# Kernel tuning notes

Measured on AMD Instinct MI355X. Metric: run time of the kernel, lower is better.

The kernel has to match this reference:

```python
import jax, jax.numpy as jnp
import numpy as np

NUM_HEADS = 12
HEAD_DIM = 64  # hidden 768 / 12


def setup_inputs() -> dict:
    key = jax.random.key(0)
    k1, k2, k3, k4 = jax.random.split(key, 4)
    B, S, H = 8, 1024, 768
    scale = 1.0 / np.sqrt(H)
    hidden_states = jax.random.normal(k1, (B, S, H), dtype=jnp.float32)
    Wq = jax.random.normal(k2, (H, H), dtype=jnp.float32) * scale
    Wk = jax.random.normal(k3, (H, H), dtype=jnp.float32) * scale
    Wv = jax.random.normal(k4, (H, H), dtype=jnp.float32) * scale
    return {"hidden_states": hidden_states, "Wq": Wq, "Wk": Wk, "Wv": Wv}


def reference(hidden_states, Wq, Wk, Wv):
    B, S, H = hidden_states.shape
    nh, hd = NUM_HEADS, HEAD_DIM
    # Linear projections, no bias. torch Linear: x @ W.T with W of shape [out, in];
    # here weights are stored [out, in] == [H, H].
    def proj(W):
        y = jnp.einsum('bsh,oh->bso', hidden_states, W)
        return y.reshape(B, S, nh, hd).transpose(0, 2, 1, 3)  # [B, nh, S, hd]
    q = proj(Wq)
    k = proj(Wk)
    v = proj(Wv)
    scale = 1.0 / np.sqrt(hd).astype(np.float32)
    scores = jnp.einsum('bhqd,bhkd->bhqk', q, k) * scale  # [B, nh, S, S]
    probs = jax.nn.softmax(scores, axis=-1)
    ctx = jnp.einsum('bhqk,bhkd->bhqd', probs, v)  # [B, nh, S, hd]
    ctx = ctx.transpose(0, 2, 1, 3).reshape(B, S, nh * hd)  # [B, S, H]
    return ctx
```

## Files before the change

### kernel.cpp

```cpp
#include <hip/hip_runtime.h>
#include <hip/hip_fp16.h>

typedef _Float16 f16;
typedef _Float16 f16x2 __attribute__((ext_vector_type(2)));
typedef _Float16 f16x4 __attribute__((ext_vector_type(4)));
typedef _Float16 f16x8 __attribute__((ext_vector_type(8)));
typedef float f32x4 __attribute__((ext_vector_type(4)));

#define GLB_AS __attribute__((address_space(1)))
#define LDS_AS __attribute__((address_space(3)))

__device__ __forceinline__ void gload_lds16(const f16* g, f16* lds) {
    __builtin_amdgcn_global_load_lds((const GLB_AS uint32_t*)g,
                                     (LDS_AS uint32_t*)lds, 16, 0, 0);
}

__device__ __forceinline__ int swz(int r, int c8) {
    return r * 64 + (((c8) ^ (r & 7)) << 3);
}

__global__ void cvt_all(const float* __restrict__ hs, const float* __restrict__ wq,
                        const float* __restrict__ wk, const float* __restrict__ wv,
                        f16* __restrict__ hs16, f16* __restrict__ w16) {
    int i = blockIdx.x * 256 + threadIdx.x;
    const float4* src;
    f16x4* dst;
    int off;
    if (i < 1572864) {
        src = (const float4*)hs; dst = (f16x4*)hs16; off = i;
    } else {
        int j = i - 1572864;
        int w = j / 147456;
        off = j - w * 147456;
        src = (const float4*)(w == 0 ? wq : (w == 1 ? wk : wv));
        dst = (f16x4*)(w16 + (size_t)w * 589824);
    }
    float4 v = src[off];
    f16x4 h = {(f16)v.x, (f16)v.y, (f16)v.z, (f16)v.w};
    dst[off] = h;
}

#define QSCALE 0.18033688011112043f

__global__ __launch_bounds__(256, 3) void qkv_gemm(
        const f16* __restrict__ A, const f16* __restrict__ W,
        f16* __restrict__ Qh, f16* __restrict__ Kh, f16* __restrict__ Vth) {
    __shared__ f16 As[128 * 64];
    __shared__ f16 Bs[128 * 64];
    const int m0 = blockIdx.x * 128;
    const int n0 = blockIdx.y * 128;
    const int tid = threadIdx.x;
    const int wave = tid >> 6, lane = tid & 63;
    const int wm = wave & 1, wn = wave >> 1;
    const int quad = lane >> 4, l16 = lane & 15;
    const int srow = lane >> 3;
    const int scol = (((lane & 7) ^ srow) << 3);

    f32x4 acc[4][4] = {};

    const f16* Abase = A + (size_t)m0 * 768;
    const f16* Wbase = W + (size_t)n0 * 768;

    for (int kt = 0; kt < 12; ++kt) {
        const int k0 = kt * 64;
        __syncthreads();
#pragma unroll
        for (int j = 0; j < 4; ++j) {
            int inst = wave * 4 + j;
            int row = inst * 8 + srow;
            gload_lds16(Abase + (size_t)row * 768 + k0 + scol, &As[inst * 512]);
            gload_lds16(Wbase + (size_t)row * 768 + k0 + scol, &Bs[inst * 512]);
        }
        __syncthreads();
#pragma unroll
        for (int kk = 0; kk < 2; ++kk) {
            f16x8 af[4], bf[4];
#pragma unroll
            for (int mi = 0; mi < 4; ++mi) {
                int r = wm * 64 + mi * 16 + l16;
                af[mi] = *(const f16x8*)&As[swz(r, kk * 4 + quad)];
            }
#pragma unroll
            for (int ni = 0; ni < 4; ++ni) {
                int r = wn * 64 + ni * 16 + l16;
                bf[ni] = *(const f16x8*)&Bs[swz(r, kk * 4 + quad)];
            }
#pragma unroll
            for (int mi = 0; mi < 4; ++mi)
#pragma unroll
                for (int ni = 0; ni < 4; ++ni)
                    acc[mi][ni] = __builtin_amdgcn_mfma_f32_16x16x32_f16(
                        af[mi], bf[ni], acc[mi][ni], 0, 0, 0);
        }
    }

    const int seg = n0 / 768;
    const int obase = n0 - seg * 768;
    const float scale = (seg == 0) ? QSCALE : 1.0f;
#pragma unroll
    for (int mi = 0; mi < 4; ++mi) {
#pragma unroll
        for (int ni = 0; ni < 4; ++ni) {
            int o = obase + wn * 64 + ni * 16 + l16;
            int h = o >> 6, d = o & 63;
            if (seg == 2) {
                int gm0 = m0 + wm * 64 + mi * 16 + quad * 4;
                int b = gm0 >> 10, s = gm0 & 1023;
                size_t bh = (size_t)(b * 12 + h);
                f16x4 v4 = {(f16)acc[mi][ni][0], (f16)acc[mi][ni][1],
                            (f16)acc[mi][ni][2], (f16)acc[mi][ni][3]};
                *(f16x4*)&Vth[(bh << 16) + ((size_t)d << 10) + s] = v4;
            } else {
                f16* dst = (seg == 0) ? Qh : Kh;
#pragma unroll
                for (int r = 0; r < 4; ++r) {
                    int gm = m0 + wm * 64 + mi * 16 + quad * 4 + r;
                    int b = gm >> 10, s = gm & 1023;
                    size_t bh = (size_t)(b * 12 + h);
                    dst[((bh << 10 | s) << 6) + d] = (f16)(acc[mi][ni][r] * scale);
                }
            }
        }
    }
}

__global__ __launch_bounds__(256, 3) void attn(
        const f16* __restrict__ Qh, const f16* __restrict__ Kh,
        const f16* __restrict__ Vth, float* __restrict__ out) {
    __shared__ f16 QsPt[128 * 64];
    __shared__ f16 Ks[2][64 * 64];
    __shared__ f16 Vts[2][64 * 64];
    const int bh = blockIdx.x;
    const int q0 = blockIdx.y * 128;
    const int b = bh / 12, h = bh % 12;
    const int tid = threadIdx.x, wave = tid >> 6, lane = tid & 63;
    const int quad = lane >> 4, l16 = lane & 15;
    const int srow = lane >> 3;
    const int scol = (((lane & 7) ^ srow) << 3);

    const f16* qbase = Qh + ((size_t)bh * 1024 + q0) * 64;
    const f16* kbase = Kh + (size_t)bh * 1024 * 64;
    const f16* vtbase = Vth + (size_t)bh * 64 * 1024;

#pragma unroll
    for (int j = 0; j < 4; ++j) {
        int inst = wave * 4 + j;
        int row = inst * 8 + srow;
        gload_lds16(qbase + row * 64 + scol, &QsPt[inst * 512]);
    }
#pragma unroll
    for (int j = 0; j < 2; ++j) {
        int inst = wave * 2 + j;
        int row = inst * 8 + srow;
        gload_lds16(kbase + (size_t)row * 64 + scol, &Ks[0][inst * 512]);
        gload_lds16(vtbase + (size_t)row * 1024 + scol, &Vts[0][inst * 512]);
    }
    __syncthreads();

    f16x8 qa[2][2];
#pragma unroll
    for (int t = 0; t < 2; ++t)
#pragma unroll
        for (int kk = 0; kk < 2; ++kk)
            qa[t][kk] = *(const f16x8*)&QsPt[swz(wave * 32 + t * 16 + l16, kk * 4 + quad)];
    __syncthreads();

    const int ptb0 = (wave * 2 + 0) * 1024;
    const int ptb1 = (wave * 2 + 1) * 1024;
    const int rowoff = l16 * 64;

    f32x4 o_acc[2][4] = {};
    float rsum[2] = {0.f, 0.f};

    for (int kb = 0; kb < 16; ++kb) {
        const int cur = kb & 1;
        if (kb < 15) {
            const int nk0 = (kb + 1) * 64;
#pragma unroll
            for (int j = 0; j < 2; ++j) {
                int inst = wave * 2 + j;
                int row = inst * 8 + srow;
                gload_lds16(kbase + (size_t)(nk0 + row) * 64 + scol,
                            &Ks[cur ^ 1][inst * 512]);
                gload_lds16(vtbase + (size_t)row * 1024 + nk0 + scol,
                            &Vts[cur ^ 1][inst * 512]);
            }
        }

        f32x4 st[2][4] = {};
#pragma unroll
        for (int kk = 0; kk < 2; ++kk) {
            f16x8 kf[4];
#pragma unroll
            for (int ct = 0; ct < 4; ++ct)
                kf[ct] = *(const f16x8*)&Ks[cur][swz(ct * 16 + l16, kk * 4 + quad)];
#pragma unroll
            for (int t = 0; t < 2; ++t)
#pragma unroll
                for (int ct = 0; ct < 4; ++ct)
                    st[t][ct] = __builtin_amdgcn_mfma_f32_16x16x32_f16(
                        kf[ct], qa[t][kk], st[t][ct], 0, 0, 0);
        }

#pragma unroll
        for (int t = 0; t < 2; ++t) {
            const int ptb = t ? ptb1 : ptb0;
#pragma unroll
            for (int ct = 0; ct < 4; ++ct) {
                float e0 = __builtin_amdgcn_exp2f(st[t][ct][0]);
                float e1 = __builtin_amdgcn_exp2f(st[t][ct][1]);
                float e2 = __builtin_amdgcn_exp2f(st[t][ct][2]);
                float e3 = __builtin_amdgcn_exp2f(st[t][ct][3]);
                rsum[t] += (e0 + e1) + (e2 + e3);
                f16x4 pv = {(f16)e0, (f16)e1, (f16)e2, (f16)e3};
                *(f16x4*)&QsPt[ptb + rowoff + (((ct * 4 + quad) ^ l16) << 2)] = pv;
            }
        }

#pragma unroll
        for (int kk = 0; kk < 2; ++kk) {
            f16x8 vf[4];
#pragma unroll
            for (int ct = 0; ct < 4; ++ct)
                vf[ct] = *(const f16x8*)&Vts[cur][swz(ct * 16 + l16, kk * 4 + quad)];
#pragma unroll
            for (int t = 0; t < 2; ++t) {
                const int ptb = t ? ptb1 : ptb0;
                int s8 = kk * 8 + quad * 2;
                f16x4 plo = *(const f16x4*)&QsPt[ptb + rowoff + ((s8 ^ l16) << 2)];
                f16x4 phi = *(const f16x4*)&QsPt[ptb + rowoff + (((s8 + 1) ^ l16) << 2)];
                f16x8 pa = {plo.x, plo.y, plo.z, plo.w, phi.x, phi.y, phi.z, phi.w};
#pragma unroll
                for (int ct = 0; ct < 4; ++ct)
                    o_acc[t][ct] = __builtin_amdgcn_mfma_f32_16x16x32_f16(
                        pa, vf[ct], o_acc[t][ct], 0, 0, 0);
            }
        }

        if (kb < 15) __syncthreads();
    }

#pragma unroll
    for (int t = 0; t < 2; ++t) {
        float rt = rsum[t];
        rt += __shfl_xor(rt, 16, 64);
        rt += __shfl_xor(rt, 32, 64);
        float rv[4];
#pragma unroll
        for (int r = 0; r < 4; ++r)
            rv[r] = 1.0f / __shfl(rt, quad * 4 + r, 64);
#pragma unroll
        for (int ct = 0; ct < 4; ++ct)
#pragma unroll
            for (int r = 0; r < 4; ++r) {
                int s = q0 + wave * 32 + t * 16 + quad * 4 + r;
                int d = ct * 16 + l16;
                out[((size_t)b * 1024 + s) * 768 + (size_t)h * 64 + d] =
                    o_acc[t][ct][r] * rv[r];
            }
    }
}

extern "C" void kernel_launch(void* const* d_in, const int* in_sizes, int n_in,
                              void* d_out, int out_size, void* d_ws, size_t ws_size,
                              hipStream_t stream) {
    const float* hs = (const float*)d_in[0];
    const float* Wq = (const float*)d_in[1];
    const float* Wk = (const float*)d_in[2];
    const float* Wv = (const float*)d_in[3];
    float* out = (float*)d_out;

    char* ws = (char*)d_ws;
    f16* hs16 = (f16*)ws;
    f16* w16  = (f16*)(ws + 12582912);
    f16* Qh   = (f16*)(ws + 16121856);
    f16* Kh   = (f16*)(ws + 28704768);
    f16* Vth  = (f16*)(ws + 41287680);

    cvt_all<<<7872, 256, 0, stream>>>(hs, Wq, Wk, Wv, hs16, w16);
    qkv_gemm<<<dim3(64, 18), 256, 0, stream>>>(hs16, w16, Qh, Kh, Vth);
    attn<<<dim3(96, 8), 256, 0, stream>>>(Qh, Kh, Vth, out);
    (void)in_sizes; (void)n_in; (void)out_size; (void)ws_size;
}
```

Baseline: 160.6 us.

## Split attention key dimension across waves with in-register P and LDS reduction

The attention kernel now gives each block 64 queries instead of 128 and splits each 64-key tile across the four waves (16 keys per wave), so every wave handles all queries. The exp'd scores are fed straight from registers into 16x16x16 MFMAs against V, which removes the LDS round-trip for P. Partial outputs and row sums are then combined across waves through an LDS reduction in the epilogue. The grid doubles to 1536 blocks for better occupancy, at the cost of more K/V reloads per query, the extra cross-wave reduction and synchronisation, and a larger o_acc register footprint.

Result: slower. 228.6 us (+42.3%).

```diff
diff --git a/kernel.cpp b/kernel.cpp
--- a/kernel.cpp
+++ b/kernel.cpp
@@ -2,7 +2,6 @@
 #include <hip/hip_fp16.h>
 
 typedef _Float16 f16;
-typedef _Float16 f16x2 __attribute__((ext_vector_type(2)));
 typedef _Float16 f16x4 __attribute__((ext_vector_type(4)));
 typedef _Float16 f16x8 __attribute__((ext_vector_type(8)));
 typedef float f32x4 __attribute__((ext_vector_type(4)));
@@ -127,12 +126,17 @@
 __global__ __launch_bounds__(256, 3) void attn(
         const f16* __restrict__ Qh, const f16* __restrict__ Kh,
         const f16* __restrict__ Vth, float* __restrict__ out) {
-    __shared__ f16 QsPt[128 * 64];
-    __shared__ f16 Ks[2][64 * 64];
-    __shared__ f16 Vts[2][64 * 64];
+    __shared__ __align__(16) char smem[42240];
+    f16* Qs = (f16*)smem;
+    f16* Ks = (f16*)(smem + 8192);
+    f16* Vts = (f16*)(smem + 24576);
+    float* red = (float*)smem;
+    float* rbuf = (float*)(smem + 40960);
+    float* dbuf = (float*)(smem + 41984);
+
     const int bh = blockIdx.x;
-    const int q0 = blockIdx.y * 128;
-    const int b = bh / 12, h = bh % 12;
+    const int q0 = blockIdx.y * 64;
+    const int b = bh / 12, hh = bh % 12;
     const int tid = threadIdx.x, wave = tid >> 6, lane = tid & 63;
     const int quad = lane >> 4, l16 = lane & 15;
     const int srow = lane >> 3;
@@ -143,34 +147,27 @@
     const f16* vtbase = Vth + (size_t)bh * 64 * 1024;
 
 #pragma unroll
-    for (int j = 0; j < 4; ++j) {
-        int inst = wave * 4 + j;
-        int row = inst * 8 + srow;
-        gload_lds16(qbase + row * 64 + scol, &QsPt[inst * 512]);
-    }
-#pragma unroll
     for (int j = 0; j < 2; ++j) {
         int inst = wave * 2 + j;
         int row = inst * 8 + srow;
-        gload_lds16(kbase + (size_t)row * 64 + scol, &Ks[0][inst * 512]);
-        gload_lds16(vtbase + (size_t)row * 1024 + scol, &Vts[0][inst * 512]);
-    }
-    __syncthreads();
-
-    f16x8 qa[2][2];
-#pragma unroll
-    for (int t = 0; t < 2; ++t)
+        gload_lds16(qbase + row * 64 + scol, &Qs[inst * 512]);
+        gload_lds16(kbase + (size_t)row * 64 + scol, &Ks[inst * 512]);
+        gload_lds16(vtbase + (size_t)row * 1024 + scol, &Vts[inst * 512]);
+    }
+    __syncthreads();
+
+    f16x8 qf[4][2];
+#pragma unroll
+    for (int t = 0; t < 4; ++t)
 #pragma unroll
         for (int kk = 0; kk < 2; ++kk)
-            qa[t][kk] = *(const f16x8*)&QsPt[swz(wave * 32 + t * 16 + l16, kk * 4 + quad)];
-    __syncthreads();
-
-    const int ptb0 = (wave * 2 + 0) * 1024;
-    const int ptb1 = (wave * 2 + 1) * 1024;
-    const int rowoff = l16 * 64;
-
-    f32x4 o_acc[2][4] = {};
-    float rsum[2] = {0.f, 0.f};
+            qf[t][kk] = *(const f16x8*)&Qs[swz(t * 16 + l16, kk * 4 + quad)];
+
+    const int vc8 = wave * 2 + (quad >> 1);
+    const int vrem = (quad & 1) * 4;
+
+    f32x4 o_acc[4][4] = {};
+    f32x4 rs = {0.f, 0.f, 0.f, 0.f};
 
     for (int kb = 0; kb < 16; ++kb) {
         const int cur = kb & 1;
@@ -181,83 +178,103 @@
                 int inst = wave * 2 + j;
                 int row = inst * 8 + srow;
                 gload_lds16(kbase + (size_t)(nk0 + row) * 64 + scol,
-                            &Ks[cur ^ 1][inst * 512]);
+                            &Ks[(cur ^ 1) * 4096 + inst * 512]);
                 gload_lds16(vtbase + (size_t)row * 1024 + nk0 + scol,
-                            &Vts[cur ^ 1][inst * 512]);
+                            &Vts[(cur ^ 1) * 4096 + inst * 512]);
             }
         }
 
-        f32x4 st[2][4] = {};
-#pragma unroll
-        for (int kk = 0; kk < 2; ++kk) {
-            f16x8 kf[4];
+        f16x8 af0 = *(const f16x8*)&Ks[cur * 4096 + swz(wave * 16 + l16, quad)];
+        f16x8 af1 = *(const f16x8*)&Ks[cur * 4096 + swz(wave * 16 + l16, 4 + quad)];
+
+        f16x4 vf[4];
+#pragma unroll
+        for (int ct = 0; ct < 4; ++ct) {
+            int r = ct * 16 + l16;
+            vf[ct] = *(const f16x4*)&Vts[cur * 4096 + r * 64 +
+                                         ((vc8 ^ (r & 7)) << 3) + vrem];
+        }
+
+#pragma unroll
+        for (int t = 0; t < 4; ++t) {
+            f32x4 st = {};
+            st = __builtin_amdgcn_mfma_f32_16x16x32_f16(af0, qf[t][0], st, 0, 0, 0);
+            st = __builtin_amdgcn_mfma_f32_16x16x32_f16(af1, qf[t][1], st, 0, 0, 0);
+            float e0 = __builtin_amdgcn_exp2f(st[0]);
+            float e1 = __builtin_amdgcn_exp2f(st[1]);
+            float e2 = __builtin_amdgcn_exp2f(st[2]);
+            float e3 = __builtin_amdgcn_exp2f(st[3]);
+            rs[t] += (e0 + e1) + (e2 + e3);
+            f16x4 pv = {(f16)e0, (f16)e1, (f16)e2, (f16)e3};
 #pragma unroll
             for (int ct = 0; ct < 4; ++ct)
-                kf[ct] = *(const f16x8*)&Ks[cur][swz(ct * 16 + l16, kk * 4 + quad)];
-#pragma unroll
-            for (int t = 0; t < 2; ++t)
-#pragma unroll
-                for (int ct = 0; ct < 4; ++ct)
-                    st[t][ct] = __builtin_amdgcn_mfma_f32_16x16x32_f16(
-                        kf[ct], qa[t][kk], st[t][ct], 0, 0, 0);
-        }
-
-#pragma unroll
-        for (int t = 0; t < 2; ++t) {
-            const int ptb = t ? ptb1 : ptb0;
-#pragma unroll
-            for (int ct = 0; ct < 4; ++ct) {
-                float e0 = __builtin_amdgcn_exp2f(st[t][ct][0]);
-                float e1 = __builtin_amdgcn_exp2f(st[t][ct][1]);
-                float e2 = __builtin_amdgcn_exp2f(st[t][ct][2]);
-                float e3 = __builtin_amdgcn_exp2f(st[t][ct][3]);
-                rsum[t] += (e0 + e1) + (e2 + e3);
-                f16x4 pv = {(f16)e0, (f16)e1, (f16)e2, (f16)e3};
-                *(f16x4*)&QsPt[ptb + rowoff + (((ct * 4 + quad) ^ l16) << 2)] = pv;
-            }
-        }
-
-#pragma unroll
-        for (int kk = 0; kk < 2; ++kk) {
-            f16x8 vf[4];
-#pragma unroll
-            for (int ct = 0; ct < 4; ++ct)
-                vf[ct] = *(const f16x8*)&Vts[cur][swz(ct * 16 + l16, kk * 4 + quad)];
-#pragma unroll
-            for (int t = 0; t < 2; ++t) {
-                const int ptb = t ? ptb1 : ptb0;
-                int s8 = kk * 8 + quad * 2;
-                f16x4 plo = *(const f16x4*)&QsPt[ptb + rowoff + ((s8 ^ l16) << 2)];
-                f16x4 phi = *(const f16x4*)&QsPt[ptb + rowoff + (((s8 + 1) ^ l16) << 2)];
-                f16x8 pa = {plo.x, plo.y, plo.z, plo.w, phi.x, phi.y, phi.z, phi.w};
-#pragma unroll
-                for (int ct = 0; ct < 4; ++ct)
-                    o_acc[t][ct] = __builtin_amdgcn_mfma_f32_16x16x32_f16(
-                        pa, vf[ct], o_acc[t][ct], 0, 0, 0);
-            }
+                o_acc[t][ct] = __builtin_amdgcn_mfma_f32_16x16x16f16(
+                    pv, vf[ct], o_acc[t][ct], 0, 0, 0);
         }
 
         if (kb < 15) __syncthreads();
     }
 
-#pragma unroll
-    for (int t = 0; t < 2; ++t) {
-        float rt = rsum[t];
+    __syncthreads();
+
+#pragma unroll
+    for (int t = 0; t < 4; ++t) {
+        float rt = rs[t];
         rt += __shfl_xor(rt, 16, 64);
         rt += __shfl_xor(rt, 32, 64);
-        float rv[4];
-#pragma unroll
-        for (int r = 0; r < 4; ++r)
-            rv[r] = 1.0f / __shfl(rt, quad * 4 + r, 64);
+        if (quad == 0) rbuf[wave * 64 + t * 16 + l16] = rt;
+    }
+#pragma unroll
+    for (int t = 0; t < 2; ++t)
 #pragma unroll
         for (int ct = 0; ct < 4; ++ct)
-#pragma unroll
-            for (int r = 0; r < 4; ++r) {
-                int s = q0 + wave * 32 + t * 16 + quad * 4 + r;
-                int d = ct * 16 + l16;
-                out[((size_t)b * 1024 + s) * 768 + (size_t)h * 64 + d] =
-                    o_acc[t][ct][r] * rv[r];
-            }
+            *(f32x4*)&red[(wave * 64 + ct * 16 + l16) * 36 + (t & 1) * 16 + quad * 4] =
+                o_acc[t][ct];
+    __syncthreads();
+    if (tid < 64) {
+        float s = rbuf[tid] + rbuf[64 + tid] + rbuf[128 + tid] + rbuf[192 + tid];
+        dbuf[tid] = 1.0f / s;
+    }
+    __syncthreads();
+
+    const int d = tid & 63, qq0 = (tid >> 6) * 8;
+    {
+        f32x4 s0 = {}, s1 = {};
+#pragma unroll
+        for (int w = 0; w < 4; ++w) {
+            s0 += *(const f32x4*)&red[(w * 64 + d) * 36 + qq0];
+            s1 += *(const f32x4*)&red[(w * 64 + d) * 36 + qq0 + 4];
+        }
+#pragma unroll
+        for (int j = 0; j < 4; ++j) {
+            out[((size_t)b * 1024 + q0 + qq0 + j) * 768 + hh * 64 + d] =
+                s0[j] * dbuf[qq0 + j];
+            out[((size_t)b * 1024 + q0 + qq0 + 4 + j) * 768 + hh * 64 + d] =
+                s1[j] * dbuf[qq0 + 4 + j];
+        }
+    }
+    __syncthreads();
+#pragma unroll
+    for (int t = 2; t < 4; ++t)
+#pragma unroll
+        for (int ct = 0; ct < 4; ++ct)
+            *(f32x4*)&red[(wave * 64 + ct * 16 + l16) * 36 + (t & 1) * 16 + quad * 4] =
+                o_acc[t][ct];
+    __syncthreads();
+    {
+        f32x4 s0 = {}, s1 = {};
+#pragma unroll
+        for (int w = 0; w < 4; ++w) {
+            s0 += *(const f32x4*)&red[(w * 64 + d) * 36 + qq0];
+            s1 += *(const f32x4*)&red[(w * 64 + d) * 36 + qq0 + 4];
+        }
+#pragma unroll
+        for (int j = 0; j < 4; ++j) {
+            out[((size_t)b * 1024 + q0 + 32 + qq0 + j) * 768 + hh * 64 + d] =
+                s0[j] * dbuf[32 + qq0 + j];
+            out[((size_t)b * 1024 + q0 + 32 + qq0 + 4 + j) * 768 + hh * 64 + d] =
+                s1[j] * dbuf[32 + qq0 + 4 + j];
+        }
     }
 }
 
@@ -279,6 +296,6 @@
 
     cvt_all<<<7872, 256, 0, stream>>>(hs, Wq, Wk, Wv, hs16, w16);
     qkv_gemm<<<dim3(64, 18), 256, 0, stream>>>(hs16, w16, Qh, Kh, Vth);
-    attn<<<dim3(96, 8), 256, 0, stream>>>(Qh, Kh, Vth, out);
+    attn<<<dim3(96, 16), 256, 0, stream>>>(Qh, Kh, Vth, out);
     (void)in_sizes; (void)n_in; (void)out_size; (void)ws_size;
 }
```
